# Performance work log

Hardware: AMD Instinct MI355X
Metric: run time of the kernel (lower is better)

The kernel has to match this reference:

```python
import jax, jax.numpy as jnp
from jax import lax
import numpy as np

B, T, N, D = 16, 2048, 8, 512


def _div_term(d):
    # exp(arange(0,d,2) * -(ln 10000)/d), as in FixedEmbedding
    return jnp.exp(jnp.arange(0, d, 2).astype(jnp.float32) * (-np.log(10000.0) / d))


def _fixed_table(c, d):
    pos = jnp.arange(c, dtype=jnp.float32)[:, None]
    ang = pos * _div_term(d)  # [c, d/2]
    tab = jnp.zeros((c, d), dtype=jnp.float32)
    tab = tab.at[:, 0::2].set(jnp.sin(ang)).at[:, 1::2].set(jnp.cos(ang))
    return tab


def setup_inputs() -> dict:
    key = jax.random.key(0)
    k1, k2, k3 = jax.random.split(key, 3)
    x = jax.random.normal(k1, (B, T, N), dtype=jnp.float32)
    x_mark = jax.random.randint(k2, (B, T, 4), 0, 7).astype(jnp.int64)
    conv_w = jax.random.normal(k3, (D, N, 3), dtype=jnp.float32) * 0.05
    return {"x": x, "x_mark": x_mark, "conv_w": conv_w}


def reference(x, x_mark, conv_w):
    b, t, n = x.shape
    d = conv_w.shape[0]

    # --- TokenEmbedding: Conv1d(c_in->d_model, k=3, circular padding, no bias) ---
    xp = jnp.transpose(x, (0, 2, 1))  # [b, n, t]
    xpad = jnp.concatenate([xp[..., -1:], xp, xp[..., :1]], axis=-1)  # circular pad 1
    val = lax.conv_general_dilated(
        xpad, conv_w, window_strides=(1,), padding="VALID",
        dimension_numbers=("NCH", "OIH", "NCH"))  # [b, d, t]
    val = jnp.transpose(val, (0, 2, 1))  # [b, t, d]

    # --- TemporalEmbedding (fixed sinusoidal tables), freq='h' ---
    # columns: 0=month(<13), 1=day(<32), 2=weekday(<7), 3=hour(<24)
    temp = (_fixed_table(24, d)[x_mark[:, :, 3]]
            + _fixed_table(7, d)[x_mark[:, :, 2]]
            + _fixed_table(32, d)[x_mark[:, :, 1]]
            + _fixed_table(13, d)[x_mark[:, :, 0]])  # [b, t, d]

    # --- Cycle_PositionalEmbedding (k=1) ---
    fft_abs = jnp.abs(jnp.fft.rfft(x, axis=1))  # [b, t//2+1, n]
    top_idx = jnp.argmax(fft_abs, axis=1)  # [b, n]; topk(k=1) == argmax (first max)
    freqs = jnp.fft.fftfreq(t, d=1.0)  # length t; rfft indices are in range
    periods = jnp.clip(t / freqs[top_idx], 1.0, float(t))  # [b, n]; 0-freq -> inf -> t
    time_idx = jnp.arange(t, dtype=jnp.float32)[None, :, None]  # [1, t, 1]
    pidx = jnp.floor(time_idx % periods[:, None, :])  # [b, t, n] (.long() truncation)

    # FixedEmbedding row for index p is sin/cos(p*div) independent of c_in
    ang = pidx[..., None] * _div_term(d)  # [b, t, n, d/2]
    pe = jnp.stack([jnp.sin(ang), jnp.cos(ang)], axis=-1).reshape(b, t, n, d)
    cyc = pe.mean(axis=2)  # [b, t, d]

    # dropout is identity in eval mode
    return val + temp + cyc
```

## Files before the change

kernel.cpp:

```cpp
#include <hip/hip_runtime.h>
#include <math.h>

#define B_ 16
#define T_ 2048
#define N_ 8
#define D_ 512
#define DTW 4
#define LPAD 520

#define NEG_W0 (-3.0679615757712823e-3f)
#define NEG_LDIV (-0.035977892078031555f)

typedef __attribute__((ext_vector_type(8))) short bf16x8;
typedef __attribute__((ext_vector_type(4))) float f32x4;

static __device__ __forceinline__ short f2bf(float f) {
  unsigned int u = __float_as_uint(f);
  unsigned int r = u + 0x7FFFu + ((u >> 16) & 1u);
  return (short)(r >> 16);
}


__global__ __launch_bounds__(512) void prep_kernel(
    const float* __restrict__ x, const int* __restrict__ xmark,
    const float* __restrict__ convw, float* __restrict__ pmax,
    float* __restrict__ nyqS, float* __restrict__ tab,
    short* __restrict__ amat, short* __restrict__ xbf,
    short* __restrict__ cnt) {
  __shared__ __align__(16) float2 zs[1088];
  __shared__ __align__(16) float2 tws[544];
  __shared__ float red[8];
  int tid = threadIdx.x;
  int blk = blockIdx.x;

  if (blk < 128) {
    int bn = blk;
    int b = bn >> 3, n = bn & 7;
    const float* xb = x + (size_t)b * (T_ * N_) + n;

    {
      float ss, cc;
      sincosf((float)tid * (2.0f * NEG_W0), &ss, &cc);
      tws[tid + (tid >> 4)] = make_float2(cc, ss);
    }
#pragma unroll
    for (int u = 0; u < 2; ++u) {
      int tau = tid + u * 512;
      float re = xb[(2 * tau) * 8];
      float im = xb[(2 * tau + 1) * 8];
      int p = __brev(tau) >> 22;
      zs[p + (p >> 4)] = make_float2(re, im);
    }
    __syncthreads();

#pragma unroll
    for (int s = 1; s <= 10; ++s) {
      int half = 1 << (s - 1);
      int idx = tid & (half - 1);
      int grp = tid >> (s - 1);
      int p0 = grp * (half << 1) + idx;
      int p1 = p0 + half;
      int ti = idx << (10 - s);
      float2 tw = tws[ti + (ti >> 4)];
      float2 a = zs[p0 + (p0 >> 4)];
      float2 bv = zs[p1 + (p1 >> 4)];
      float tr = bv.x * tw.x - bv.y * tw.y;
      float tq = fmaf(bv.x, tw.y, bv.y * tw.x);
      zs[p1 + (p1 >> 4)] = make_float2(a.x - tr, a.y - tq);
      zs[p0 + (p0 >> 4)] = make_float2(a.x + tr, a.y + tq);
      __syncthreads();
    }

    int j = tid;
    int jm = (1024 - j) & 1023;
    float2 A = zs[j + (j >> 4)];
    float2 Bv = zs[jm + (jm >> 4)];
    float u = A.x - Bv.x, v = A.y + Bv.y;
    float Ere = 0.5f * (A.x + Bv.x), Eim = 0.5f * (A.y - Bv.y);
    float Ore = 0.5f * v, Oim = -0.5f * u;
    float cw, sw;
    sincosf((float)j * NEG_W0, &sw, &cw);
    float Gr = Ere + cw * Ore - sw * Oim;
    float Gi = Eim + cw * Oim + sw * Ore;
    float P = fmaf(Gr, Gr, Gi * Gi);
    float Gpr = Ere - cw * Ore + sw * Oim;
    float Gpi = -Eim + cw * Oim + sw * Ore;
    float P2;
    if (j == 0) {
      nyqS[bn] = Gpr;
      float2 Am = zs[512 + (512 >> 4)];
      P2 = fmaf(Am.x, Am.x, Am.y * Am.y);
    } else {
      P2 = fmaf(Gpr, Gpr, Gpi * Gpi);
    }
    P = fmaxf(P, P2);
#pragma unroll
    for (int off = 32; off > 0; off >>= 1) P = fmaxf(P, __shfl_down(P, off));
    if ((tid & 63) == 0) red[tid >> 6] = P;
    __syncthreads();
    if (tid == 0) {
      float mx = red[0];
#pragma unroll
      for (int k = 1; k < 8; ++k) mx = fmaxf(mx, red[k]);
      pmax[bn] = mx;
    }
    return;
  }

  int j = blk - 128;
  if (j < 32) {
    int gt = j * 512 + tid;
    int tb = gt >> 7;
    int d4 = gt & 127;
    float dv0 = expf((float)(d4 * 2) * NEG_LDIV);
    float dv1 = expf((float)(d4 * 2 + 1) * NEG_LDIV);
    float tf = (float)(tb * 16);
    float s0, c0, s1, c1, r0s, r0c, r1s, r1c;
    sincosf(tf * dv0, &s0, &c0);
    sincosf(tf * dv1, &s1, &c1);
    sincosf(dv0, &r0s, &r0c);
    sincosf(dv1, &r1s, &r1c);
    float* row = tab + (size_t)(tb * 16) * D_ + d4 * 4;
#pragma unroll
    for (int u = 0; u < 16; ++u) {
      f32x4 v; v[0] = s0; v[1] = c0; v[2] = s1; v[3] = c1;
      *(f32x4*)row = v;
      row += D_;
      float ns0 = fmaf(s0, r0c, c0 * r0s), nc0 = fmaf(c0, r0c, -s0 * r0s);
      s0 = ns0; c0 = nc0;
      float ns1 = fmaf(s1, r1c, c1 * r1s), nc1 = fmaf(c1, r1c, -s1 * r1s);
      s1 = ns1; c1 = nc1;
    }
  } else if (j < 96) {
    int r = (j - 32) * 512 + tid;
    const float4* xr = (const float4*)(x + (size_t)r * 8);
    float4 lo = xr[0], hi = xr[1];
    bf16x8 v;
    v[0] = f2bf(lo.x); v[1] = f2bf(lo.y); v[2] = f2bf(lo.z); v[3] = f2bf(lo.w);
    v[4] = f2bf(hi.x); v[5] = f2bf(hi.y); v[6] = f2bf(hi.z); v[7] = f2bf(hi.w);
    *(bf16x8*)(xbf + (size_t)r * 8) = v;
    int4 mk = *(const int4*)(xmark + (size_t)r * 4);
    bf16x8 cv;
#pragma unroll
    for (int p = 0; p < 8; ++p) {
      int cc = (mk.x == p) + (mk.y == p) + (mk.z == p) + (mk.w == p);
      cv[p] = f2bf((float)cc);
    }
    *(bf16x8*)(cnt + (size_t)r * 8) = cv;
  } else {
    int d = tid;
    short row[32];
#pragma unroll
    for (int kk = 0; kk < 24; ++kk) {
      int g = kk >> 3, n = kk & 7;
      row[kk] = f2bf(convw[d * 24 + n * 3 + g]);
    }
    float divv = expf((float)(d >> 1) * NEG_LDIV);
    float s1, c1;
    sincosf(divv, &s1, &c1);
    int odd = d & 1;
    row[24] = f2bf(odd ? 1.f : 0.f);
    float ps = s1, pc = c1;
    row[25] = f2bf(odd ? pc : ps);
#pragma unroll
    for (int p = 2; p < 7; ++p) {
      float ns = fmaf(ps, c1, pc * s1);
      float nc = fmaf(pc, c1, -ps * s1);
      ps = ns; pc = nc;
      row[24 + p] = f2bf(odd ? pc : ps);
    }
    row[31] = 0;
#pragma unroll
    for (int q = 0; q < 4; ++q)
      *(bf16x8*)(amat + d * 32 + q * 8) = *(bf16x8*)&row[q * 8];
  }
}

__global__ __launch_bounds__(512, 6) void main_kernel(
    const short* __restrict__ amat, const short* __restrict__ xbf,
    const short* __restrict__ cnt, const float* __restrict__ tab,
    const float* __restrict__ pmax, const float* __restrict__ nyqS,
    float* __restrict__ out) {
  __shared__ __align__(16) float lds[16 * LPAD];
  int tid = threadIdx.x;
  int lane = tid & 63;
  int w = tid >> 6;
  int c = lane & 15;
  int g = lane >> 4;
  int blk = blockIdx.x;
  int ttile = blk & 127;
  int bg = blk >> 7;
  int t0 = ttile * 16;

  float w1v[2], w0v[2];
#pragma unroll
  for (int j = 0; j < 2; ++j) {
    int b = bg * 2 + j;
    int m = 0;
#pragma unroll
    for (int nn = 0; nn < 8; ++nn) {
      int bn = b * 8 + nn;
      float mx = pmax[bn];
      float S = nyqS[bn];
      if (S * S > mx) ++m;
    }
    w1v[j] = (float)(8 - m) * 0.125f;
    w0v[j] = (float)m * 0.125f;
  }

  bf16x8 afrag[DTW];
  f32x4 fet[DTW];
#pragma unroll
  for (int q = 0; q < DTW; ++q) {
    int d0 = (w * DTW + q) * 16;
    afrag[q] = *(const bf16x8*)(amat + (size_t)(d0 + c) * 32 + g * 8);
    fet[q] = *(const f32x4*)(tab + (size_t)(t0 + c) * D_ + d0 + g * 4);
  }

  const f32x4 zac = {0.f, 0.f, 0.f, 0.f};
#pragma unroll
  for (int j = 0; j < 2; ++j) {
    int b = bg * 2 + j;
    bf16x8 bfrag;
    if (g < 3) {
      int row = (t0 + c + g - 1) & (T_ - 1);
      bfrag = *(const bf16x8*)(xbf + ((size_t)b * T_ + row) * 8);
    } else {
      bfrag = *(const bf16x8*)(cnt + ((size_t)b * T_ + t0 + c) * 8);
    }
    float w1 = w1v[j], w0 = w0v[j];
#pragma unroll
    for (int q = 0; q < DTW; ++q) {
      f32x4 acc = __builtin_amdgcn_mfma_f32_16x16x32_bf16(
          afrag[q], bfrag, zac, 0, 0, 0);
      f32x4 ov;
      ov[0] = fmaf(w1, fet[q][0], acc[0]);
      ov[1] = fmaf(w1, fet[q][1], acc[1]) + w0;
      ov[2] = fmaf(w1, fet[q][2], acc[2]);
      ov[3] = fmaf(w1, fet[q][3], acc[3]) + w0;
      int d0 = (w * DTW + q) * 16;
      *(f32x4*)(lds + c * LPAD + d0 + g * 4) = ov;
    }
    __syncthreads();
    float* obase = out + ((size_t)b * T_ + t0) * D_;
#pragma unroll
    for (int r = 0; r < 4; ++r) {
      int e = r * 2048 + tid * 4;
      int trow = e >> 9, col = e & 511;
      f32x4 v = *(const f32x4*)(lds + trow * LPAD + col);
      *(f32x4*)(obase + e) = v;
    }
    if (j == 0) __syncthreads();
  }
}

extern "C" void kernel_launch(void* const* d_in, const int* in_sizes, int n_in,
                              void* d_out, int out_size, void* d_ws, size_t ws_size,
                              hipStream_t stream) {
  const float* x = (const float*)d_in[0];
  const int* xmark = (const int*)d_in[1];
  const float* convw = (const float*)d_in[2];
  float* out = (float*)d_out;

  char* ws = (char*)d_ws;
  float* pmax = (float*)ws;
  float* nyqS = (float*)(ws + 2048);
  float* tab = (float*)(ws + 8192);
  short* amat = (short*)(ws + 8192 + 4194304);
  short* xbf = (short*)(ws + 8192 + 4194304 + 32768);
  short* cnt = (short*)(ws + 8192 + 4194304 + 32768 + 524288);

  prep_kernel<<<225, 512, 0, stream>>>(x, xmark, convw, pmax, nyqS, tab,
                                       amat, xbf, cnt);
  main_kernel<<<(T_ / 16) * (B_ / 2), 512, 0, stream>>>(amat, xbf, cnt, tab,
                                                        pmax, nyqS, out);
}
```

Before: 27.11 us.

## Split main kernel over D halves and compute sinusoid table directly per row

The main kernel now uses 256-thread blocks that each cover half of the D dimension, which doubles the grid to 2048 blocks and halves the LDS staging tile. The A fragments are loaded inside the MFMA loop instead of being held in registers. The prep kernel now fills the positional table with 128 blocks that call sincos directly for every element, replacing the 32-block rotation recurrence. This gives more parallelism and occupancy in both kernels, at the cost of extra transcendental work and some extra launch and block overhead.

```diff
diff --git a/kernel.cpp b/kernel.cpp
--- a/kernel.cpp
+++ b/kernel.cpp
@@ -5,8 +5,7 @@
 #define T_ 2048
 #define N_ 8
 #define D_ 512
-#define DTW 4
-#define LPAD 520
+#define LP2 264
 
 #define NEG_W0 (-3.0679615757712823e-3f)
 #define NEG_LDIV (-0.035977892078031555f)
@@ -108,31 +107,25 @@
   }
 
   int j = blk - 128;
-  if (j < 32) {
-    int gt = j * 512 + tid;
-    int tb = gt >> 7;
-    int d4 = gt & 127;
-    float dv0 = expf((float)(d4 * 2) * NEG_LDIV);
-    float dv1 = expf((float)(d4 * 2 + 1) * NEG_LDIV);
-    float tf = (float)(tb * 16);
-    float s0, c0, s1, c1, r0s, r0c, r1s, r1c;
-    sincosf(tf * dv0, &s0, &c0);
-    sincosf(tf * dv1, &s1, &c1);
-    sincosf(dv0, &r0s, &r0c);
-    sincosf(dv1, &r1s, &r1c);
-    float* row = tab + (size_t)(tb * 16) * D_ + d4 * 4;
-#pragma unroll
-    for (int u = 0; u < 16; ++u) {
-      f32x4 v; v[0] = s0; v[1] = c0; v[2] = s1; v[3] = c1;
-      *(f32x4*)row = v;
-      row += D_;
-      float ns0 = fmaf(s0, r0c, c0 * r0s), nc0 = fmaf(c0, r0c, -s0 * r0s);
-      s0 = ns0; c0 = nc0;
-      float ns1 = fmaf(s1, r1c, c1 * r1s), nc1 = fmaf(c1, r1c, -s1 * r1s);
-      s1 = ns1; c1 = nc1;
-    }
-  } else if (j < 96) {
-    int r = (j - 32) * 512 + tid;
+  if (j < 128) {
+    int base = j * 2048 + tid * 4;
+#pragma unroll
+    for (int u = 0; u < 4; ++u) {
+      int idx = base + u;
+      int t = idx >> 7;
+      int d4 = idx & 127;
+      float ft = (float)t;
+      float dv0 = expf((float)(d4 * 2) * NEG_LDIV);
+      float dv1 = expf((float)(d4 * 2 + 1) * NEG_LDIV);
+      f32x4 v;
+      float s0, c0, s1, c1;
+      sincosf(ft * dv0, &s0, &c0);
+      sincosf(ft * dv1, &s1, &c1);
+      v[0] = s0; v[1] = c0; v[2] = s1; v[3] = c1;
+      *(f32x4*)(tab + (size_t)idx * 4) = v;
+    }
+  } else if (j < 192) {
+    int r = (j - 128) * 512 + tid;
     const float4* xr = (const float4*)(x + (size_t)r * 8);
     float4 lo = xr[0], hi = xr[1];
     bf16x8 v;
@@ -176,12 +169,12 @@
   }
 }
 
-__global__ __launch_bounds__(512, 6) void main_kernel(
+__global__ __launch_bounds__(256, 8) void main_kernel(
     const short* __restrict__ amat, const short* __restrict__ xbf,
     const short* __restrict__ cnt, const float* __restrict__ tab,
     const float* __restrict__ pmax, const float* __restrict__ nyqS,
     float* __restrict__ out) {
-  __shared__ __align__(16) float lds[16 * LPAD];
+  __shared__ __align__(16) float lds[16 * LP2];
   int tid = threadIdx.x;
   int lane = tid & 63;
   int w = tid >> 6;
@@ -189,8 +182,11 @@
   int g = lane >> 4;
   int blk = blockIdx.x;
   int ttile = blk & 127;
-  int bg = blk >> 7;
+  int rest = blk >> 7;
+  int bg = rest & 7;
+  int dhalf = rest >> 3;
   int t0 = ttile * 16;
+  int dbase = dhalf * 256;
 
   float w1v[2], w0v[2];
 #pragma unroll
@@ -208,13 +204,11 @@
     w0v[j] = (float)m * 0.125f;
   }
 
-  bf16x8 afrag[DTW];
-  f32x4 fet[DTW];
-#pragma unroll
-  for (int q = 0; q < DTW; ++q) {
-    int d0 = (w * DTW + q) * 16;
-    afrag[q] = *(const bf16x8*)(amat + (size_t)(d0 + c) * 32 + g * 8);
-    fet[q] = *(const f32x4*)(tab + (size_t)(t0 + c) * D_ + d0 + g * 4);
+  f32x4 fet[4];
+#pragma unroll
+  for (int q = 0; q < 4; ++q) {
+    int dq = dbase + (w * 4 + q) * 16;
+    fet[q] = *(const f32x4*)(tab + (size_t)(t0 + c) * D_ + dq + g * 4);
   }
 
   const f32x4 zac = {0.f, 0.f, 0.f, 0.f};
@@ -230,25 +224,26 @@
     }
     float w1 = w1v[j], w0 = w0v[j];
 #pragma unroll
-    for (int q = 0; q < DTW; ++q) {
+    for (int q = 0; q < 4; ++q) {
+      int dq = dbase + (w * 4 + q) * 16;
+      bf16x8 afrag = *(const bf16x8*)(amat + (size_t)(dq + c) * 32 + g * 8);
       f32x4 acc = __builtin_amdgcn_mfma_f32_16x16x32_bf16(
-          afrag[q], bfrag, zac, 0, 0, 0);
+          afrag, bfrag, zac, 0, 0, 0);
       f32x4 ov;
       ov[0] = fmaf(w1, fet[q][0], acc[0]);
       ov[1] = fmaf(w1, fet[q][1], acc[1]) + w0;
       ov[2] = fmaf(w1, fet[q][2], acc[2]);
       ov[3] = fmaf(w1, fet[q][3], acc[3]) + w0;
-      int d0 = (w * DTW + q) * 16;
-      *(f32x4*)(lds + c * LPAD + d0 + g * 4) = ov;
+      *(f32x4*)(lds + c * LP2 + (w * 4 + q) * 16 + g * 4) = ov;
     }
     __syncthreads();
-    float* obase = out + ((size_t)b * T_ + t0) * D_;
+    float* obase = out + ((size_t)b * T_ + t0) * D_ + dbase;
 #pragma unroll
     for (int r = 0; r < 4; ++r) {
-      int e = r * 2048 + tid * 4;
-      int trow = e >> 9, col = e & 511;
-      f32x4 v = *(const f32x4*)(lds + trow * LPAD + col);
-      *(f32x4*)(obase + e) = v;
+      int e = r * 1024 + tid * 4;
+      int trow = e >> 8, col = e & 255;
+      f32x4 v = *(const f32x4*)(lds + trow * LP2 + col);
+      *(f32x4*)(obase + trow * D_ + col) = v;
     }
     if (j == 0) __syncthreads();
   }
@@ -270,8 +265,7 @@
   short* xbf = (short*)(ws + 8192 + 4194304 + 32768);
   short* cnt = (short*)(ws + 8192 + 4194304 + 32768 + 524288);
 
-  prep_kernel<<<225, 512, 0, stream>>>(x, xmark, convw, pmax, nyqS, tab,
+  prep_kernel<<<321, 512, 0, stream>>>(x, xmark, convw, pmax, nyqS, tab,
                                        amat, xbf, cnt);
-  main_kernel<<<(T_ / 16) * (B_ / 2), 512, 0, stream>>>(amat, xbf, cnt, tab,
-                                                        pmax, nyqS, out);
-}
+  main_kernel<<<2048, 256, 0, stream>>>(amat, xbf, cnt, tab, pmax, nyqS, out);
+}
```

Result: faster. 25.99 us, median of 2 (-4.1%).
